# Kernel tuning notes

Hardware: AMD Instinct MI355X
Metric: run time of the kernel (lower is better)

Reference implementation:

```python
import jax, jax.numpy as jnp
import numpy as np

CTX = 2048
D_IN = 2048
D_OUT = 2048
N_HEADS = 16
HEAD_DIM = D_OUT // N_HEADS
ROPE_BASE = 10000.0


def rope_tables(head_dim, ctx):
    inv_freq = 1.0 / (ROPE_BASE ** (jnp.arange(0, head_dim, 2, dtype=jnp.float32) / head_dim))
    angles = jnp.arange(ctx, dtype=jnp.float32)[:, None] * inv_freq[None, :]  # [ctx, hd/2]
    angles = jnp.concatenate([angles, angles], axis=1)  # [ctx, hd]
    return jnp.sin(angles), jnp.cos(angles)


def apply_rope(x, sin, cos):
    # x: [b, h, s, d]; rotate-by-half (Raschka / Llama style)
    s = x.shape[2]
    d = x.shape[3]
    x1, x2 = x[..., : d // 2], x[..., d // 2 :]
    rotated = jnp.concatenate([-x2, x1], axis=-1)
    return x * cos[:s][None, None] + rotated * sin[:s][None, None]


def setup_inputs() -> dict:
    key = jax.random.key(0)
    kx, kq, kk, kv, ko = jax.random.split(key, 5)
    scale = 0.02
    return {
        "x": jax.random.normal(kx, (2, CTX, D_IN), dtype=jnp.float32),
        "W_query": jax.random.normal(kq, (D_IN, D_OUT), dtype=jnp.float32) * scale,
        "W_key": jax.random.normal(kk, (D_IN, D_OUT), dtype=jnp.float32) * scale,
        "W_value": jax.random.normal(kv, (D_IN, D_OUT), dtype=jnp.float32) * scale,
        "W_out": jax.random.normal(ko, (D_OUT, D_OUT), dtype=jnp.float32) * scale,
    }


def reference(x, W_query, W_key, W_value, W_out):
    bs, cl, _ = x.shape
    sin, cos = rope_tables(HEAD_DIM, CTX)

    def split_heads(t):  # [b, s, d_out] -> [b, h, s, hd]
        return t.reshape(bs, cl, N_HEADS, HEAD_DIM).transpose(0, 2, 1, 3)

    q = split_heads(x @ W_query)
    k = split_heads(x @ W_key)
    v = split_heads(x @ W_value)

    q = apply_rope(q, sin, cos)
    k = apply_rope(k, sin, cos)

    # NOTE: original module does NOT scale by 1/sqrt(head_dim)
    scores = jnp.einsum("bhqd,bhkd->bhqk", q, k)
    causal = jnp.triu(jnp.ones((cl, cl), dtype=bool), k=1)
    scores = jnp.where(causal[None, None], -jnp.inf, scores)
    weights = jax.nn.softmax(scores, axis=-1)
    ctx = jnp.einsum("bhqk,bhkd->bhqd", weights, v)
    ctx = ctx.transpose(0, 2, 1, 3).reshape(bs, cl, N_HEADS * HEAD_DIM)
    return ctx @ W_out
```

## Files before the change

kernel.cpp:

```cpp
#include <hip/hip_runtime.h>
#include <cstdint>
#include <cstddef>

typedef _Float16 f16;
typedef _Float16 f16x8 __attribute__((ext_vector_type(8)));
typedef _Float16 f16x4 __attribute__((ext_vector_type(4)));
typedef float    f32x4 __attribute__((ext_vector_type(4)));
typedef float    f32x16 __attribute__((ext_vector_type(16)));
typedef int      i32x4 __attribute__((ext_vector_type(4)));

#define S_CTX 2048
#define NH 16
#define DH 128

#define BAR() asm volatile("s_barrier" ::: "memory")
#define VMW(n) asm volatile("s_waitcnt vmcnt(" #n ")" ::: "memory")
#define MF(a, b, c) __builtin_amdgcn_mfma_f32_16x16x32_f16((a), (b), (c), 0, 0, 0)
#define MF32(a, b, c) __builtin_amdgcn_mfma_f32_32x32x16_f16((a), (b), (c), 0, 0, 0)

__device__ __forceinline__ void gload16(const void* g, void* l) {
  __builtin_amdgcn_global_load_lds(
      (const __attribute__((address_space(1))) void*)g,
      (__attribute__((address_space(3))) void*)l, 16, 0, 0);
}

__device__ __forceinline__ int pk2(float a, float b) {
  auto hv = __builtin_amdgcn_cvt_pkrtz(a, b);
  return __builtin_bit_cast(int, hv);
}
__device__ __forceinline__ void pl_swap(int& a, int& b) {
  asm volatile("v_permlane32_swap_b32 %0, %1" : "+v"(a), "+v"(b));
}

__global__ void prep(const float* __restrict__ x,
                     const float* __restrict__ w0, const float* __restrict__ w1,
                     const float* __restrict__ w2, const float* __restrict__ w3,
                     f16* __restrict__ xb,
                     f16* __restrict__ o0, f16* __restrict__ o1,
                     f16* __restrict__ o2, f16* __restrict__ o3,
                     float* __restrict__ sint, float* __restrict__ cost) {
  const int bid = blockIdx.x, tid = threadIdx.x;
  if (bid < 512) {
    int idx = bid * 256 + tid;
    int j = idx & 63, s = idx >> 6;
    float invf = __expf(-(float)(2 * j) * (1.0f / 128.0f) * 9.210340371976184f);
    float a = (float)s * invf;
    sint[idx] = sinf(a);
    cost[idx] = cosf(a);
  } else if (bid < 8704) {
    int i = ((bid - 512) * 256 + tid) * 4;
    float4 v = *(const float4*)(x + i);
    f16x4 o; o[0] = (f16)v.x; o[1] = (f16)v.y; o[2] = (f16)v.z; o[3] = (f16)v.w;
    *(f16x4*)(xb + i) = o;
  } else {
    int b2 = bid - 8704;
    int z = b2 >> 12, rem = b2 & 4095;
    int by = rem >> 6, bx = rem & 63;
    int tx = tid & 31, ty = tid >> 5;
    const float* in; f16* out;
    switch (z) {
      case 0: in = w0; out = o0; break;
      case 1: in = w1; out = o1; break;
      case 2: in = w2; out = o2; break;
      default: in = w3; out = o3; break;
    }
    __shared__ float tl[32][33];
    int xc = bx * 32 + tx, yc = by * 32 + ty;
#pragma unroll
    for (int r = 0; r < 32; r += 8)
      tl[ty + r][tx] = in[(size_t)(yc + r) * 2048 + xc];
    __syncthreads();
    int xo = by * 32 + tx, yo = bx * 32 + ty;
#pragma unroll
    for (int r = 0; r < 32; r += 8)
      out[(size_t)(yo + r) * 2048 + xo] = (f16)tl[tx][ty + r];
  }
}

__global__ __launch_bounds__(512, 1)
void gemm_qk(const f16* __restrict__ A, const f16* __restrict__ wqT,
             const f16* __restrict__ wkT,
             f16* __restrict__ qb, f16* __restrict__ kb,
             const float* __restrict__ sint, const float* __restrict__ cost) {
  extern __shared__ __align__(16) char lds[];
  const int tid = threadIdx.x, lane = tid & 63;
  const int wvi = tid >> 6, wm = wvi >> 2, wn = wvi & 3;
  const int gcol = blockIdx.x * 256;
  const int proj = gcol >> 11;
  const int col0 = gcol & 2047;
  const int row0 = blockIdx.y * 256;
  const f16* Bt = proj ? wkT : wqT;

  const int ca0 = tid, ca1 = tid + 512;
  const int ra0 = ca0 >> 2, ra1 = ca1 >> 2;
  const int sa0 = (ca0 & 3) ^ ((ra0 >> 1) & 3);
  const int sa1 = (ca1 & 3) ^ ((ra1 >> 1) & 3);
  const f16* gA0 = A + (size_t)(row0 + ra0) * 2048 + sa0 * 8;
  const f16* gA1 = A + (size_t)(row0 + ra1) * 2048 + sa1 * 8;
  const f16* gB0 = Bt + (size_t)(col0 + ra0) * 2048 + sa0 * 8;
  const f16* gB1 = Bt + (size_t)(col0 + ra1) * 2048 + sa1 * 8;

  const int kslot = lane >> 4;
  int aoff[8], boff[4];
#pragma unroll
  for (int i = 0; i < 8; i++) {
    int row = wm * 128 + i * 16 + (lane & 15);
    aoff[i] = row * 64 + ((kslot ^ ((row >> 1) & 3)) << 4);
  }
#pragma unroll
  for (int j = 0; j < 4; j++) {
    int rb = (wn >> 1) * 128 + (wn & 1) * 32 + (j & 1) * 16 + (j >> 1) * 64 + (lane & 15);
    boff[j] = rb * 64 + ((kslot ^ ((rb >> 1) & 3)) << 4);
  }

  f32x4 acc[8][4] = {};

#define QKPH(SLOT, HS, SSLOT, DOSTAGE, WN) do {                                \
    const char* As_ = lds + (SLOT) * 32768;                                    \
    const char* Bs_ = As_ + 16384;                                             \
    f16x8 af[8], bf[4];                                                        \
    _Pragma("unroll") for (int i_ = 0; i_ < 8; i_++)                           \
      af[i_] = *(const f16x8*)(As_ + aoff[i_]);                                \
    _Pragma("unroll") for (int j_ = 0; j_ < 4; j_++)                           \
      bf[j_] = *(const f16x8*)(Bs_ + boff[j_]);                                \
    if (DOSTAGE) {                                                             \
      char* dA = lds + (SSLOT) * 32768;                                        \
      gload16(gA0 + (HS) * 32, dA + ca0 * 16);                                 \
      gload16(gA1 + (HS) * 32, dA + ca1 * 16);                                 \
      gload16(gB0 + (HS) * 32, dA + 16384 + ca0 * 16);                         \
      gload16(gB1 + (HS) * 32, dA + 16384 + ca1 * 16);                         \
    }                                                                          \
    asm volatile("s_waitcnt vmcnt(" #WN ")" ::: "memory");                     \
    BAR();                                                                     \
    __builtin_amdgcn_s_setprio(1);                                             \
    _Pragma("unroll") for (int i_ = 0; i_ < 8; i_++)                           \
      _Pragma("unroll") for (int j_ = 0; j_ < 4; j_++)                         \
        acc[i_][j_] = MF(af[i_], bf[j_], acc[i_][j_]);                         \
    __builtin_amdgcn_s_setprio(0);                                             \
    BAR();                                                                     \
  } while (0)

#pragma unroll
  for (int h = 0; h < 2; h++) {
    char* dA = lds + h * 32768;
    gload16(gA0 + h * 32, dA + ca0 * 16);
    gload16(gA1 + h * 32, dA + ca1 * 16);
    gload16(gB0 + h * 32, dA + 16384 + ca0 * 16);
    gload16(gB1 + h * 32, dA + 16384 + ca1 * 16);
  }
  VMW(4); BAR();

  for (int t = 0; t < 20; ++t) {
    const int hb = 3 * t;
    QKPH(0, hb + 2, 2, 1, 4);
    QKPH(1, hb + 3, 0, 1, 4);
    QKPH(2, hb + 4, 1, 1, 4);
  }
  QKPH(0, 62, 2, 1, 4);
  QKPH(1, 63, 0, 1, 4);
  QKPH(2, 0, 0, 0, 0);
  QKPH(0, 0, 0, 0, 63);
#undef QKPH

  const int b = row0 >> 11, sb = row0 & 2047;
  f16* dst = proj ? kb : qb;
  const int h = (col0 >> 7) + (wn >> 1);
#pragma unroll
  for (int i = 0; i < 8; i++)
#pragma unroll
    for (int jj = 0; jj < 2; jj++)
#pragma unroll
      for (int r = 0; r < 4; r++) {
        int s = sb + wm * 128 + i * 16 + (lane >> 4) * 4 + r;
        int d = (wn & 1) * 32 + jj * 16 + (lane & 15);
        float cv = cost[s * 64 + d], sv = sint[s * 64 + d];
        float x1 = acc[i][jj][r], x2 = acc[i][jj + 2][r];
        size_t base = ((size_t)(b * NH + h) * S_CTX + s) << 7;
        dst[base + d]      = (f16)(x1 * cv - x2 * sv);
        dst[base + d + 64] = (f16)(x2 * cv + x1 * sv);
      }
}

template<int MODE>
__global__ __launch_bounds__(512, 1)
void gemm8(const f16* __restrict__ A, const f16* __restrict__ Bt,
           f16* __restrict__ vtb, float* __restrict__ of) {
  extern __shared__ __align__(16) char lds[];
#define RING_A(e) (lds + (e) * 16384)
#define RING_B(e) (lds + 65536 + (e) * 8192)
  const int tid = threadIdx.x, lane = tid & 63;
  const int wvi = tid >> 6, wm = wvi >> 1, wn = wvi & 1;
  const int col0 = blockIdx.x * 128;
  const int row0 = blockIdx.y * 256;

  const int ca0 = tid, ca1 = tid + 512, cb0 = tid;
  const int rAs0 = ca0 >> 2, rAs1 = ca1 >> 2, rBs0 = cb0 >> 2;
  const int sA0 = (ca0 & 3) ^ ((rAs0 >> 1) & 3);
  const int sA1 = (ca1 & 3) ^ ((rAs1 >> 1) & 3);
  const int sB0 = (cb0 & 3) ^ ((rBs0 >> 1) & 3);
  const f16* gA0 = A + (size_t)(row0 + rAs0) * 2048 + sA0 * 8;
  const f16* gA1 = A + (size_t)(row0 + rAs1) * 2048 + sA1 * 8;
  const f16* gB0 = Bt + (size_t)(col0 + rBs0) * 2048 + sB0 * 8;

  const int kslot = lane >> 4;
  int aoff[4], boff[4];
#pragma unroll
  for (int i = 0; i < 4; i++) {
    int row = wm * 64 + i * 16 + (lane & 15);
    aoff[i] = row * 64 + ((kslot ^ ((row >> 1) & 3)) << 4);
  }
#pragma unroll
  for (int j = 0; j < 4; j++) {
    int rb = wn * 32 + (j & 1) * 16 + (j >> 1) * 64 + (lane & 15);
    boff[j] = rb * 64 + ((kslot ^ ((rb >> 1) & 3)) << 4);
  }

  f32x4 acc[4][4] = {};

#define PH8(SLOT, HS, DOSTAGE, WN) do {                                        \
    const char* As_ = RING_A(SLOT);                                            \
    const char* Bs_ = RING_B(SLOT);                                            \
    f16x8 af[4], bf[4];                                                        \
    _Pragma("unroll") for (int i_ = 0; i_ < 4; i_++)                           \
      af[i_] = *(const f16x8*)(As_ + aoff[i_]);                                \
    _Pragma("unroll") for (int j_ = 0; j_ < 4; j_++)                           \
      bf[j_] = *(const f16x8*)(Bs_ + boff[j_]);                                \
    if (DOSTAGE) {                                                             \
      gload16(gA0 + (HS) * 32, RING_A((HS) & 3) + ca0 * 16);                   \
      gload16(gA1 + (HS) * 32, RING_A((HS) & 3) + ca1 * 16);                   \
      gload16(gB0 + (HS) * 32, RING_B((HS) & 3) + cb0 * 16);                   \
    }                                                                          \
    asm volatile("s_waitcnt vmcnt(" #WN ")" ::: "memory");                     \
    BAR();                                                                     \
    __builtin_amdgcn_s_setprio(1);                                             \
    _Pragma("unroll") for (int i_ = 0; i_ < 4; i_++)                           \
      _Pragma("unroll") for (int j_ = 0; j_ < 4; j_++)                         \
        acc[i_][j_] = MF(af[i_], bf[j_], acc[i_][j_]);                         \
    __builtin_amdgcn_s_setprio(0);                                             \
    BAR();                                                                     \
  } while (0)

#pragma unroll
  for (int h = 0; h < 3; h++) {
    gload16(gA0 + h * 32, RING_A(h) + ca0 * 16);
    gload16(gA1 + h * 32, RING_A(h) + ca1 * 16);
    gload16(gB0 + h * 32, RING_B(h) + cb0 * 16);
  }
  VMW(6); BAR();

  for (int t = 0; t < 15; ++t) {
    const int p = t * 4;
    PH8(0, p + 3, 1, 6);
    PH8(1, p + 4, 1, 6);
    PH8(2, p + 5, 1, 6);
    PH8(3, p + 6, 1, 6);
  }
  PH8(0, 63, 1, 6);
  PH8(1, 0, 0, 3);
  PH8(2, 0, 0, 0);
  PH8(3, 0, 0, 63);
#undef PH8

  const int b = row0 >> 11, sbase = row0 & 2047;

  if (MODE == 2) {
#pragma unroll
    for (int i = 0; i < 4; i++)
#pragma unroll
      for (int j = 0; j < 4; j++)
#pragma unroll
        for (int r = 0; r < 4; r++) {
          int row = row0 + wm * 64 + i * 16 + (lane >> 4) * 4 + r;
          int col = col0 + wn * 32 + (j & 1) * 16 + (j >> 1) * 64 + (lane & 15);
          of[(size_t)row * 2048 + col] = acc[i][j][r];
        }
  } else {
    const int h = col0 >> 7;
    f16x4* ldsv = (f16x4*)lds;
#pragma unroll
    for (int i = 0; i < 4; i++)
#pragma unroll
      for (int j = 0; j < 4; j++) {
        f16x4 v;
#pragma unroll
        for (int r = 0; r < 4; r++) v[r] = (f16)acc[i][j][r];
        int su = wm * 16 + i * 4 + (lane >> 4);
        int d  = wn * 32 + (j & 1) * 16 + (j >> 1) * 64 + (lane & 15);
        ldsv[d * 64 + (su ^ ((d << 1) & 63))] = v;
      }
    __syncthreads();
#pragma unroll
    for (int it = 0; it < 8; ++it) {
      int o = it * 512 + tid;
      int d = o >> 5, c = o & 31;
      int xc = (d << 1) & 63;
      f16x4 lo = ldsv[d * 64 + ((2 * c) ^ xc)];
      f16x4 hi = ldsv[d * 64 + ((2 * c + 1) ^ xc)];
      f16x8 vv;
      vv[0] = lo[0]; vv[1] = lo[1]; vv[2] = lo[2]; vv[3] = lo[3];
      vv[4] = hi[0]; vv[5] = hi[1]; vv[6] = hi[2]; vv[7] = hi[3];
      *(f16x8*)&vtb[((size_t)(b * NH + h) * DH + d) * S_CTX + sbase + c * 8] = vv;
    }
  }
#undef RING_A
#undef RING_B
}

__global__ __launch_bounds__(256, 2)
void attn_k(const f16* __restrict__ q, const f16* __restrict__ kk,
            const f16* __restrict__ vt, f16* __restrict__ ctx) {
  __shared__ __align__(16) f16 Ks[2][64 * 128];
  __shared__ __align__(16) f16 Vs[2][128 * 64];
  const int tid = threadIdx.x, lane = tid & 63, wv = tid >> 6;
  const int lh = lane >> 5, q31 = lane & 31;
  const int bid = blockIdx.x;
  const int half = bid >> 8, low = bid & 255;
  const int x = low & 7, rr = low >> 3;
  const int bh = x + 8 * (rr & 3);
  const int idx = rr >> 2;
  const int Q = half ? idx : (15 - idx);
  const int b = bh >> 4, h = bh & 15;
  const size_t plane = (size_t)bh * (S_CTX * DH);
  const f16* Qp = q + plane;
  const f16* Kp = kk + plane;
  const f16* Vp = vt + plane;
  const float LOG2E = 1.4426950408889634f;
  const int q0 = Q * 128;
  const int NT = 2 * Q + 2;

#define STAGE(T, BUF) do {                                                      \
    const f16* Kt = Kp + (size_t)(T) * 64 * DH;                                 \
    const f16* Vt = Vp + (size_t)(T) * 64;                                      \
    _Pragma("unroll") for (int j_ = 0; j_ < 4; j_++) {                          \
      int c = tid + j_ * 256; int rk = c >> 4;                                  \
      gload16(Kt + (size_t)rk * DH + (((c & 15) ^ (rk & 7)) * 8), &Ks[BUF][c * 8]); \
    }                                                                           \
    _Pragma("unroll") for (int j_ = 0; j_ < 4; j_++) {                          \
      int c = tid + j_ * 256; int rv = c >> 3;                                  \
      gload16(Vt + (size_t)rv * S_CTX + (((c & 7) ^ (rv & 7)) * 8), &Vs[BUF][c * 8]); \
    }                                                                           \
  } while (0)

  f16x8 qf[8];
  {
    const f16* qq = Qp + (size_t)(q0 + wv * 32 + q31) * DH + lh * 8;
#pragma unroll
    for (int s = 0; s < 8; s++) {
      qf[s] = *(const f16x8*)(qq + s * 16);
#pragma unroll
      for (int e = 0; e < 8; e++) qf[s][e] = (f16)((float)qf[s][e] * LOG2E);
    }
  }
  float m_ = -3e38f, l_ = 0.f;
  f32x16 o[4] = {};

  STAGE(0, 0);
  VMW(0); BAR();

  int cur = 0;
  for (int t = 0; t < NT; t++) {
    if (t + 1 < NT) {
      if (cur) STAGE(t + 1, 0); else STAGE(t + 1, 1);
    }
    const f16* Ksc = Ks[cur];
    const f16* Vsc = Vs[cur];

    f32x16 st0 = {}, st1 = {};
    __builtin_amdgcn_s_setprio(1);
#pragma unroll
    for (int s = 0; s < 8; s++) {
      const int r0 = q31, r1 = 32 + q31;
      f16x8 kf0 = *(const f16x8*)&Ksc[r0 * 128 + (((2 * s + lh) ^ (r0 & 7)) << 3)];
      f16x8 kf1 = *(const f16x8*)&Ksc[r1 * 128 + (((2 * s + lh) ^ (r1 & 7)) << 3)];
      st0 = MF32(kf0, qf[s], st0);
      st1 = MF32(kf1, qf[s], st1);
    }
    __builtin_amdgcn_s_setprio(0);

    if (t >= 2 * Q) {
      const int qg = q0 + wv * 32 + q31;
#pragma unroll
      for (int r = 0; r < 16; r++) {
        int kvb = t * 64 + (r & 3) + 8 * (r >> 2) + 4 * lh;
        if (kvb > qg) st0[r] = -3e38f;
        if (kvb + 32 > qg) st1[r] = -3e38f;
      }
    }
    float mx = st0[0];
#pragma unroll
    for (int r = 1; r < 16; r++) mx = fmaxf(mx, st0[r]);
#pragma unroll
    for (int r = 0; r < 16; r++) mx = fmaxf(mx, st1[r]);
    mx = fmaxf(mx, __shfl_xor(mx, 32));
    if (__any(mx > m_ + 8.0f)) {
      float nm = fmaxf(m_, mx);
      float al = __builtin_amdgcn_exp2f(m_ - nm);
      m_ = nm; l_ *= al;
#pragma unroll
      for (int r = 0; r < 16; r++) {
        float alr = __shfl(al, (r & 3) + 8 * (r >> 2) + 4 * lh);
#pragma unroll
        for (int j = 0; j < 4; j++) o[j][r] *= alr;
      }
    }
    float s_ = 0.f;
#pragma unroll
    for (int r = 0; r < 16; r++) { st0[r] = __builtin_amdgcn_exp2f(st0[r] - m_); s_ += st0[r]; }
#pragma unroll
    for (int r = 0; r < 16; r++) { st1[r] = __builtin_amdgcn_exp2f(st1[r] - m_); s_ += st1[r]; }
    s_ += __shfl_xor(s_, 32);
    l_ += s_;

    f16x8 pa[4];
    {
      int w0 = pk2(st0[0], st0[1]),   w1 = pk2(st0[2], st0[3]);
      int w2 = pk2(st0[4], st0[5]),   w3 = pk2(st0[6], st0[7]);
      int w4 = pk2(st0[8], st0[9]),   w5 = pk2(st0[10], st0[11]);
      int w6 = pk2(st0[12], st0[13]), w7 = pk2(st0[14], st0[15]);
      pl_swap(w0, w2); pl_swap(w1, w3); pl_swap(w4, w6); pl_swap(w5, w7);
      i32x4 a = {w0, w1, w2, w3}; pa[0] = __builtin_bit_cast(f16x8, a);
      i32x4 bb = {w4, w5, w6, w7}; pa[1] = __builtin_bit_cast(f16x8, bb);
    }
    {
      int w0 = pk2(st1[0], st1[1]),   w1 = pk2(st1[2], st1[3]);
      int w2 = pk2(st1[4], st1[5]),   w3 = pk2(st1[6], st1[7]);
      int w4 = pk2(st1[8], st1[9]),   w5 = pk2(st1[10], st1[11]);
      int w6 = pk2(st1[12], st1[13]), w7 = pk2(st1[14], st1[15]);
      pl_swap(w0, w2); pl_swap(w1, w3); pl_swap(w4, w6); pl_swap(w5, w7);
      i32x4 a = {w0, w1, w2, w3}; pa[2] = __builtin_bit_cast(f16x8, a);
      i32x4 bb = {w4, w5, w6, w7}; pa[3] = __builtin_bit_cast(f16x8, bb);
    }

    __builtin_amdgcn_s_setprio(1);
#pragma unroll
    for (int j = 0; j < 4; j++) {
      const int rv = 32 * j + q31;
#pragma unroll
      for (int s2 = 0; s2 < 4; s2++) {
        f16x8 vf = *(const f16x8*)&Vsc[rv * 64 + (((2 * s2 + lh) ^ (rv & 7)) << 3)];
        o[j] = MF32(pa[s2], vf, o[j]);
      }
    }
    __builtin_amdgcn_s_setprio(0);

    VMW(0); BAR();
    cur ^= 1;
  }
#undef STAGE

  float inv = 1.0f / l_;
#pragma unroll
  for (int r = 0; r < 16; r++) {
    int crow = (r & 3) + 8 * (r >> 2) + 4 * lh;
    float invr = __shfl(inv, crow);
    int qg = q0 + wv * 32 + crow;
#pragma unroll
    for (int j = 0; j < 4; j++) {
      int dd = h * 128 + 32 * j + q31;
      ctx[((size_t)(b * S_CTX + qg) * 2048) + dd] = (f16)(o[j][r] * invr);
    }
  }
}

extern "C" void kernel_launch(void* const* d_in, const int* in_sizes, int n_in,
                              void* d_out, int out_size, void* d_ws, size_t ws_size,
                              hipStream_t stream) {
  (void)in_sizes; (void)n_in; (void)out_size; (void)ws_size;
  const float* x  = (const float*)d_in[0];
  const float* Wq = (const float*)d_in[1];
  const float* Wk = (const float*)d_in[2];
  const float* Wv = (const float*)d_in[3];
  const float* Wo = (const float*)d_in[4];
  float* out = (float*)d_out;
  char* ws = (char*)d_ws;

  f16*   xb   = (f16*)(ws);
  f16*   ctxb = (f16*)(ws);
  f16*   wqT  = (f16*)(ws + 16777216);
  f16*   wkT  = (f16*)(ws + 25165824);
  f16*   wvT  = (f16*)(ws + 33554432);
  f16*   woT  = (f16*)(ws + 41943040);
  f16*   qb   = (f16*)(ws + 50331648);
  f16*   kb   = (f16*)(ws + 67108864);
  f16*   vtb  = (f16*)(ws + 83886080);
  float* sint = (float*)(ws + 100663296);
  float* cost = (float*)(ws + 101187584);

  prep<<<dim3(25088), dim3(256), 0, stream>>>(x, Wq, Wk, Wv, Wo, xb,
                                              wqT, wkT, wvT, woT, sint, cost);
  gemm_qk<<<dim3(16, 16), dim3(512), 98304, stream>>>(xb, wqT, wkT, qb, kb, sint, cost);
  gemm8<1><<<dim3(16, 16), dim3(512), 98304, stream>>>(xb, wvT, vtb, nullptr);
  attn_k<<<dim3(512), dim3(256), 0, stream>>>(qb, kb, vtb, ctxb);
  gemm8<2><<<dim3(16, 16), dim3(512), 98304, stream>>>(ctxb, woT, nullptr, out);
}
```

Before: 251.0 us.

## Process two K-slices per barrier pair in projection GEMM pipelines

```diff
diff --git a/kernel.cpp b/kernel.cpp
--- a/kernel.cpp
+++ b/kernel.cpp
@@ -115,52 +115,50 @@
 
   f32x4 acc[8][4] = {};
 
-#define QKPH(SLOT, HS, SSLOT, DOSTAGE, WN) do {                                \
-    const char* As_ = lds + (SLOT) * 32768;                                    \
+#define QKSTG(H) do {                                                          \
+    char* d_ = lds + ((H) & 3) * 32768;                                        \
+    gload16(gA0 + (H) * 32, d_ + ca0 * 16);                                    \
+    gload16(gA1 + (H) * 32, d_ + ca1 * 16);                                    \
+    gload16(gB0 + (H) * 32, d_ + 16384 + ca0 * 16);                            \
+    gload16(gB1 + (H) * 32, d_ + 16384 + ca1 * 16);                            \
+  } while (0)
+
+#define QKHALF(S) do {                                                         \
+    const char* As_ = lds + (S) * 32768;                                       \
     const char* Bs_ = As_ + 16384;                                             \
     f16x8 af[8], bf[4];                                                        \
     _Pragma("unroll") for (int i_ = 0; i_ < 8; i_++)                           \
       af[i_] = *(const f16x8*)(As_ + aoff[i_]);                                \
     _Pragma("unroll") for (int j_ = 0; j_ < 4; j_++)                           \
       bf[j_] = *(const f16x8*)(Bs_ + boff[j_]);                                \
-    if (DOSTAGE) {                                                             \
-      char* dA = lds + (SSLOT) * 32768;                                        \
-      gload16(gA0 + (HS) * 32, dA + ca0 * 16);                                 \
-      gload16(gA1 + (HS) * 32, dA + ca1 * 16);                                 \
-      gload16(gB0 + (HS) * 32, dA + 16384 + ca0 * 16);                         \
-      gload16(gB1 + (HS) * 32, dA + 16384 + ca1 * 16);                         \
-    }                                                                          \
-    asm volatile("s_waitcnt vmcnt(" #WN ")" ::: "memory");                     \
-    BAR();                                                                     \
     __builtin_amdgcn_s_setprio(1);                                             \
     _Pragma("unroll") for (int i_ = 0; i_ < 8; i_++)                           \
       _Pragma("unroll") for (int j_ = 0; j_ < 4; j_++)                         \
         acc[i_][j_] = MF(af[i_], bf[j_], acc[i_][j_]);                         \
     __builtin_amdgcn_s_setprio(0);                                             \
+  } while (0)
+
+#define QKPAIR(S0, S1, H2, H3, DOSTAGE, WN) do {                               \
+    if (DOSTAGE) { QKSTG(H2); QKSTG(H3); }                                     \
+    asm volatile("s_waitcnt vmcnt(" #WN ")" ::: "memory");                     \
     BAR();                                                                     \
-  } while (0)
-
-#pragma unroll
-  for (int h = 0; h < 2; h++) {
-    char* dA = lds + h * 32768;
-    gload16(gA0 + h * 32, dA + ca0 * 16);
-    gload16(gA1 + h * 32, dA + ca1 * 16);
-    gload16(gB0 + h * 32, dA + 16384 + ca0 * 16);
-    gload16(gB1 + h * 32, dA + 16384 + ca1 * 16);
-  }
-  VMW(4); BAR();
-
-  for (int t = 0; t < 20; ++t) {
-    const int hb = 3 * t;
-    QKPH(0, hb + 2, 2, 1, 4);
-    QKPH(1, hb + 3, 0, 1, 4);
-    QKPH(2, hb + 4, 1, 1, 4);
-  }
-  QKPH(0, 62, 2, 1, 4);
-  QKPH(1, 63, 0, 1, 4);
-  QKPH(2, 0, 0, 0, 0);
-  QKPH(0, 0, 0, 0, 63);
-#undef QKPH
+    QKHALF(S0);                                                                \
+    QKHALF(S1);                                                                \
+    BAR();                                                                     \
+  } while (0)
+
+  QKSTG(0); QKSTG(1);
+
+  for (int t = 0; t < 15; ++t) {
+    const int hb = 4 * t;
+    QKPAIR(0, 1, hb + 2, hb + 3, 1, 8);
+    QKPAIR(2, 3, hb + 4, hb + 5, 1, 8);
+  }
+  QKPAIR(0, 1, 62, 63, 1, 8);
+  QKPAIR(2, 3, 0, 0, 0, 0);
+#undef QKPAIR
+#undef QKHALF
+#undef QKSTG
 
   const int b = row0 >> 11, sb = row0 & 2047;
   f16* dst = proj ? kb : qb;
@@ -217,49 +215,48 @@
 
   f32x4 acc[4][4] = {};
 
-#define PH8(SLOT, HS, DOSTAGE, WN) do {                                        \
-    const char* As_ = RING_A(SLOT);                                            \
-    const char* Bs_ = RING_B(SLOT);                                            \
+#define G8STG(H) do {                                                          \
+    gload16(gA0 + (H) * 32, RING_A((H) & 3) + ca0 * 16);                       \
+    gload16(gA1 + (H) * 32, RING_A((H) & 3) + ca1 * 16);                       \
+    gload16(gB0 + (H) * 32, RING_B((H) & 3) + cb0 * 16);                       \
+  } while (0)
+
+#define G8HALF(S) do {                                                         \
+    const char* As_ = RING_A(S);                                               \
+    const char* Bs_ = RING_B(S);                                               \
     f16x8 af[4], bf[4];                                                        \
     _Pragma("unroll") for (int i_ = 0; i_ < 4; i_++)                           \
       af[i_] = *(const f16x8*)(As_ + aoff[i_]);                                \
     _Pragma("unroll") for (int j_ = 0; j_ < 4; j_++)                           \
       bf[j_] = *(const f16x8*)(Bs_ + boff[j_]);                                \
-    if (DOSTAGE) {                                                             \
-      gload16(gA0 + (HS) * 32, RING_A((HS) & 3) + ca0 * 16);                   \
-      gload16(gA1 + (HS) * 32, RING_A((HS) & 3) + ca1 * 16);                   \
-      gload16(gB0 + (HS) * 32, RING_B((HS) & 3) + cb0 * 16);                   \
-    }                                                                          \
-    asm volatile("s_waitcnt vmcnt(" #WN ")" ::: "memory");                     \
-    BAR();                                                                     \
     __builtin_amdgcn_s_setprio(1);                                             \
     _Pragma("unroll") for (int i_ = 0; i_ < 4; i_++)                           \
       _Pragma("unroll") for (int j_ = 0; j_ < 4; j_++)                         \
         acc[i_][j_] = MF(af[i_], bf[j_], acc[i_][j_]);                         \
     __builtin_amdgcn_s_setprio(0);                                             \
+  } while (0)
+
+#define G8PAIR(S0, S1, H2, H3, DOSTAGE, WN) do {                               \
+    if (DOSTAGE) { G8STG(H2); G8STG(H3); }                                     \
+    asm volatile("s_waitcnt vmcnt(" #WN ")" ::: "memory");                     \
     BAR();                                                                     \
-  } while (0)
-
-#pragma unroll
-  for (int h = 0; h < 3; h++) {
-    gload16(gA0 + h * 32, RING_A(h) + ca0 * 16);
-    gload16(gA1 + h * 32, RING_A(h) + ca1 * 16);
-    gload16(gB0 + h * 32, RING_B(h) + cb0 * 16);
-  }
-  VMW(6); BAR();
+    G8HALF(S0);                                                                \
+    G8HALF(S1);                                                                \
+    BAR();                                                                     \
+  } while (0)
+
+  G8STG(0); G8STG(1);
 
   for (int t = 0; t < 15; ++t) {
-    const int p = t * 4;
-    PH8(0, p + 3, 1, 6);
-    PH8(1, p + 4, 1, 6);
-    PH8(2, p + 5, 1, 6);
-    PH8(3, p + 6, 1, 6);
-  }
-  PH8(0, 63, 1, 6);
-  PH8(1, 0, 0, 3);
-  PH8(2, 0, 0, 0);
-  PH8(3, 0, 0, 63);
-#undef PH8
+    const int hb = 4 * t;
+    G8PAIR(0, 1, hb + 2, hb + 3, 1, 6);
+    G8PAIR(2, 3, hb + 4, hb + 5, 1, 6);
+  }
+  G8PAIR(0, 1, 62, 63, 1, 6);
+  G8PAIR(2, 3, 0, 0, 0, 0);
+#undef G8PAIR
+#undef G8HALF
+#undef G8STG
 
   const int b = row0 >> 11, sbase = row0 & 2047;
 
@@ -488,7 +485,7 @@
 
   prep<<<dim3(25088), dim3(256), 0, stream>>>(x, Wq, Wk, Wv, Wo, xb,
                                               wqT, wkT, wvT, woT, sint, cost);
-  gemm_qk<<<dim3(16, 16), dim3(512), 98304, stream>>>(xb, wqT, wkT, qb, kb, sint, cost);
+  gemm_qk<<<dim3(16, 16), dim3(512), 131072, stream>>>(xb, wqT, wkT, qb, kb, sint, cost);
   gemm8<1><<<dim3(16, 16), dim3(512), 98304, stream>>>(xb, wvT, vtb, nullptr);
   attn_k<<<dim3(512), dim3(256), 0, stream>>>(qb, kb, vtb, ctxb);
   gemm8<2><<<dim3(16, 16), dim3(512), 98304, stream>>>(ctxb, woT, nullptr, out);
```

Result: slower. 258.1 us (+2.8%).
